# Performance work log

Hardware: AMD Instinct MI355X
Metric: run time of the kernel (lower is better)

The kernel has to match this reference:

```python
import jax, jax.numpy as jnp
import numpy as np

NUM_Q_HEADS = 32
NUM_KV_HEADS = 8
Q_GROUP = NUM_Q_HEADS // NUM_KV_HEADS
K_DIM = 128
V_DIM = 128
EMD_DIM = 4096
ROPE_BASE = 10000.0


def _rope_tables(seq_len, dim, offset=0, dtype=jnp.float32):
    # thetas: base**(-arange(0,dim,2)/dim); ticks tiled (1,2) -> [seq,dim]
    exps = -jnp.arange(0, dim, 2, dtype=jnp.float32) / dim
    thetas = ROPE_BASE ** exps
    t = jnp.arange(offset, offset + seq_len, dtype=jnp.float32)
    ticks = jnp.outer(t, thetas)                      # [t, dim/2]
    ticks = jnp.concatenate([ticks, ticks], axis=-1)  # tile (1,2) -> [t, dim]
    ticks = ticks[None, :, None, :]                   # [1, t, 1, dim]
    return jnp.cos(ticks).astype(dtype), jnp.sin(ticks).astype(dtype)


def _apply_rope(x, cos, sin):
    # x: [B, t, H, D]; rotate-half variant: neg_half = cat(-x2, x1)
    d2 = x.shape[-1] // 2
    x1, x2 = x[..., :d2], x[..., d2:]
    neg_half = jnp.concatenate([-x2, x1], axis=-1)
    return x * cos + neg_half * sin


def setup_inputs() -> dict:
    key = jax.random.key(0)
    ks = jax.random.split(key, 7)
    B, T, D = 2, 2048, EMD_DIM
    return {
        "q": jax.random.normal(ks[0], (B, T, D), dtype=jnp.float32),
        "k": jax.random.normal(ks[1], (B, T, D), dtype=jnp.float32),
        "v": jax.random.normal(ks[2], (B, T, D), dtype=jnp.float32),
        "wq": jax.random.normal(ks[3], (D, NUM_Q_HEADS * K_DIM), dtype=jnp.float32) * 0.02,
        "wk": jax.random.normal(ks[4], (D, NUM_KV_HEADS * K_DIM), dtype=jnp.float32) * 0.02,
        "wv": jax.random.normal(ks[5], (D, NUM_KV_HEADS * V_DIM), dtype=jnp.float32) * 0.02,
        "wo": jax.random.normal(ks[6], (Q_GROUP * NUM_KV_HEADS * V_DIM, D), dtype=jnp.float32) * 0.02,
    }


def reference(q, k, v, wq, wk, wv, wo):
    B, t, D = q.shape
    cos, sin = _rope_tables(t, K_DIM, offset=0, dtype=q.dtype)

    # projections + head split (no kv_cache -> offset 0, T == t)
    q_heads = jnp.einsum('btd,de->bte', q, wq).reshape(B, t, NUM_Q_HEADS, K_DIM)
    q_heads = _apply_rope(q_heads, cos, sin)
    k_heads = jnp.einsum('btd,de->bte', k, wk).reshape(B, t, NUM_KV_HEADS, K_DIM)
    k_heads = _apply_rope(k_heads, cos, sin)
    v_heads = jnp.einsum('btd,de->bte', v, wv).reshape(B, t, NUM_KV_HEADS, V_DIM)

    # grouped attention: [B, t, G, H, K] x [B, T, H, K] -> [B, G, H, t, T]
    gq = q_heads.reshape(B, t, Q_GROUP, NUM_KV_HEADS, K_DIM)
    scores = jnp.einsum('BtGHK,BTHK->BGHtT', gq, k_heads).astype(jnp.float32)
    causal = jnp.tril(jnp.ones((t, t), dtype=bool))
    scores = jnp.where(causal, scores, -jnp.inf)
    probs = jax.nn.softmax(scores / (K_DIM ** 0.5), axis=-1).astype(v_heads.dtype)

    out = jnp.einsum('BGHtT,BTHV->BtGHV', probs, v_heads)
    out = out.reshape(B, t, Q_GROUP * NUM_KV_HEADS * V_DIM)
    out = jnp.einsum('bti,io->bto', out, wo)

    new_kv_cache = jnp.concatenate([k_heads, v_heads], axis=-1)  # [B, T, H, K+V]
    return out, new_kv_cache
```

## Files before the change

kernel.cpp:

```cpp
#include <hip/hip_runtime.h>
#include <hip/hip_bf16.h>
#include <cstdint>
#include <math.h>

#define BB 2
#define TT 2048
#define DD 4096
#define HQ 32
#define HKV 8
#define DK 128
#define MM (BB*TT)
#define NQ (HQ*DK)
#define NKV (HKV*DK)

typedef __attribute__((ext_vector_type(8))) short short8;
typedef __attribute__((ext_vector_type(4))) short bshort4;
typedef __attribute__((ext_vector_type(4))) float floatx4;

typedef unsigned int u32;
typedef __attribute__((address_space(1))) const u32 gas_u32;
typedef __attribute__((address_space(3))) u32 las_u32;

__device__ __forceinline__ void gl_lds16(const uint16_t* g, uint16_t* l) {
    __builtin_amdgcn_global_load_lds((gas_u32*)g, (las_u32*)l, 16, 0, 0);
}

__device__ inline uint16_t f2bf(float f) {
    uint32_t u = __float_as_uint(f);
    uint32_t r = (u + 0x7fffu + ((u >> 16) & 1u)) >> 16;
    return (uint16_t)r;
}

__global__ void rope_tables_k(float* __restrict__ cosT, float* __restrict__ sinT) {
    int t = blockIdx.x;
    int d = threadIdx.x;
    float theta = expf(-(float)d * (9.210340371976184f / 64.0f));
    float arg = (float)t * theta;
    float s, c;
    sincosf(arg, &s, &c);
    cosT[t * 64 + d] = c;
    sinT[t * 64 + d] = s;
}

__global__ void wconv_k(const float* __restrict__ W, uint16_t* __restrict__ WT, int K, int N) {
    __shared__ float tile[32][33];
    int n0 = blockIdx.x * 32, k0 = blockIdx.y * 32;
    int tx = threadIdx.x, ty = threadIdx.y;
#pragma unroll
    for (int i = 0; i < 4; i++) {
        int r = k0 + ty + i * 8;
        tile[ty + i * 8][tx] = W[(size_t)r * N + n0 + tx];
    }
    __syncthreads();
#pragma unroll
    for (int i = 0; i < 4; i++) {
        int r = n0 + ty + i * 8;
        WT[(size_t)r * K + k0 + tx] = f2bf(tile[tx][ty + i * 8]);
    }
}

__global__ void aconv3_k(const float4* __restrict__ Xq, const float4* __restrict__ Xk,
                         const float4* __restrict__ Xv,
                         uint2* __restrict__ Yq, uint2* __restrict__ Yk, uint2* __restrict__ Yv,
                         int n4) {
    int i = blockIdx.x * blockDim.x + threadIdx.x;
    int w = blockIdx.y;
    const float4* X = (w == 0) ? Xq : (w == 1) ? Xk : Xv;
    uint2* Y = (w == 0) ? Yq : (w == 1) ? Yk : Yv;
    if (i < n4) {
        float4 v = X[i];
        uint2 o;
        o.x = (uint32_t)f2bf(v.x) | ((uint32_t)f2bf(v.y) << 16);
        o.y = (uint32_t)f2bf(v.z) | ((uint32_t)f2bf(v.w) << 16);
        Y[i] = o;
    }
}

__device__ __forceinline__ void gemm_core(
    const uint16_t* __restrict__ A, const uint16_t* __restrict__ Bm, int K,
    int m0, int n0, int tid, uint16_t* As, uint16_t* Bs, floatx4 acc[2][8])
{
    int lane = tid & 63, wave = tid >> 6;
    int l15 = lane & 15, quad = lane >> 4;
#pragma unroll
    for (int a = 0; a < 2; a++)
#pragma unroll
        for (int b = 0; b < 8; b++) acc[a][b] = floatx4{0.f, 0.f, 0.f, 0.f};

    int srow = tid >> 3;
    int skc = (tid & 7) ^ (srow & 7);
    const uint16_t* Ag = A + (size_t)(m0 + srow) * K + skc * 8;
    const uint16_t* Bg = Bm + (size_t)(n0 + srow) * K + skc * 8;
    uint16_t* Asl = As + tid * 8;
    uint16_t* Bsl = Bs + tid * 8;
    int rswA = l15 & 7;

    for (int k0 = 0; k0 < K; k0 += 64) {
        __syncthreads();
#pragma unroll
        for (int i = 0; i < 4; i++) {
            gl_lds16(Ag + (size_t)(i * 32) * K + k0, Asl + i * 2048);
            gl_lds16(Bg + (size_t)(i * 32) * K + k0, Bsl + i * 2048);
        }
        __syncthreads();
#pragma unroll
        for (int ks = 0; ks < 2; ks++) {
            short8 af[2], bfr[8];
#pragma unroll
            for (int mt = 0; mt < 2; mt++)
                af[mt] = *(const short8*)(As + (wave * 32 + mt * 16 + l15) * 64
                                             + (((ks << 2) | quad) ^ rswA) * 8);
#pragma unroll
            for (int nt = 0; nt < 8; nt++)
                bfr[nt] = *(const short8*)(Bs + (nt * 16 + l15) * 64
                                              + (((ks << 2) | quad) ^ rswA) * 8);
#pragma unroll
            for (int mt = 0; mt < 2; mt++)
#pragma unroll
                for (int nt = 0; nt < 8; nt++)
                    acc[mt][nt] = __builtin_amdgcn_mfma_f32_16x16x32_bf16(af[mt], bfr[nt], acc[mt][nt], 0, 0, 0);
        }
    }
}

template <int EPI>
__global__ __launch_bounds__(256) void gemm_k(
    const uint16_t* __restrict__ A, const uint16_t* __restrict__ Bm,
    int M, int N, int K,
    uint16_t* __restrict__ Obf, float* __restrict__ Ofp,
    const float* __restrict__ cosT, const float* __restrict__ sinT)
{
    __shared__ __attribute__((aligned(16))) uint16_t As[128 * 64];
    __shared__ __attribute__((aligned(16))) uint16_t Bs[128 * 64];
    int m0 = blockIdx.y * 128;
    int n0 = blockIdx.x * 128;
    int tid = threadIdx.x;
    int lane = tid & 63, wave = tid >> 6;
    int l15 = lane & 15, quad = lane >> 4;

    floatx4 acc[2][8];
    gemm_core(A, Bm, K, m0, n0, tid, As, Bs, acc);

#pragma unroll
    for (int mt = 0; mt < 2; mt++) {
        int rbase = m0 + wave * 32 + mt * 16 + quad * 4;
        if (EPI == 4) {
#pragma unroll
            for (int nt = 0; nt < 8; nt++) {
                int c = n0 + nt * 16 + l15;
#pragma unroll
                for (int r = 0; r < 4; r++)
                    Ofp[(size_t)(rbase + r) * N + c] = acc[mt][nt][r];
            }
        } else {
#pragma unroll
            for (int nt = 0; nt < 4; nt++) {
                int cb = nt * 16 + l15;
#pragma unroll
                for (int r = 0; r < 4; r++) {
                    int row = rbase + r;
                    int t = row & (TT - 1);
                    float cs = cosT[t * 64 + cb];
                    float sn = sinT[t * 64 + cb];
                    float x1 = acc[mt][nt][r], x2 = acc[mt][nt + 4][r];
                    float o1 = x1 * cs - x2 * sn;
                    float o2 = x2 * cs + x1 * sn;
                    Obf[(size_t)row * N + n0 + cb] = f2bf(o1);
                    Obf[(size_t)row * N + n0 + cb + 64] = f2bf(o2);
                }
            }
        }
    }
}

__global__ __launch_bounds__(256) void gemm_kv_k(
    const uint16_t* __restrict__ Akk, const uint16_t* __restrict__ Avv,
    const uint16_t* __restrict__ Wk, const uint16_t* __restrict__ Wv,
    uint16_t* __restrict__ khB, uint16_t* __restrict__ vhB, float* __restrict__ cache,
    const float* __restrict__ cosT, const float* __restrict__ sinT)
{
    __shared__ __attribute__((aligned(16))) uint16_t As[128 * 64];
    __shared__ __attribute__((aligned(16))) uint16_t Bs[128 * 64];
    bool isK = (blockIdx.z == 1);
    const uint16_t* A = isK ? Akk : Avv;
    const uint16_t* Bm = isK ? Wk : Wv;
    int m0 = blockIdx.y * 128;
    int n0 = blockIdx.x * 128;
    int tid = threadIdx.x;
    int lane = tid & 63, wave = tid >> 6;
    int l15 = lane & 15, quad = lane >> 4;

    floatx4 acc[2][8];
    gemm_core(A, Bm, DD, m0, n0, tid, As, Bs, acc);

    int h = n0 >> 7;
#pragma unroll
    for (int mt = 0; mt < 2; mt++) {
        int rbase = m0 + wave * 32 + mt * 16 + quad * 4;
        if (!isK) {
#pragma unroll
            for (int nt = 0; nt < 8; nt++) {
                int cb = nt * 16 + l15;
#pragma unroll
                for (int r = 0; r < 4; r++) {
                    int row = rbase + r;
                    float v = acc[mt][nt][r];
                    vhB[(size_t)row * NKV + n0 + cb] = f2bf(v);
                    cache[((size_t)row * 8 + h) * 256 + 128 + cb] = v;
                }
            }
        } else {
#pragma unroll
            for (int nt = 0; nt < 4; nt++) {
                int cb = nt * 16 + l15;
#pragma unroll
                for (int r = 0; r < 4; r++) {
                    int row = rbase + r;
                    int t = row & (TT - 1);
                    float cs = cosT[t * 64 + cb];
                    float sn = sinT[t * 64 + cb];
                    float x1 = acc[mt][nt][r], x2 = acc[mt][nt + 4][r];
                    float o1 = x1 * cs - x2 * sn;
                    float o2 = x2 * cs + x1 * sn;
                    khB[(size_t)row * NKV + n0 + cb] = f2bf(o1);
                    khB[(size_t)row * NKV + n0 + cb + 64] = f2bf(o2);
                    cache[((size_t)row * 8 + h) * 256 + cb] = o1;
                    cache[((size_t)row * 8 + h) * 256 + cb + 64] = o2;
                }
            }
        }
    }
}

__global__ void vtrans_k(const uint16_t* __restrict__ vh, uint16_t* __restrict__ vT) {
    __shared__ uint16_t tile[32][33];
    int bh = blockIdx.z;
    int t0 = blockIdx.x * 32;
    int d0 = blockIdx.y * 32;
    int b = bh >> 3, h = bh & 7;
    int tx = threadIdx.x, ty = threadIdx.y;
#pragma unroll
    for (int i = 0; i < 4; i++) {
        int t = t0 + ty + i * 8;
        tile[ty + i * 8][tx] = vh[(size_t)(b * TT + t) * NKV + h * DK + d0 + tx];
    }
    __syncthreads();
#pragma unroll
    for (int i = 0; i < 4; i++) {
        int d = d0 + ty + i * 8;
        vT[((size_t)bh * DK + d) * TT + t0 + tx] = tile[tx][ty + i * 8];
    }
}

__global__ __launch_bounds__(512, 4) void attn_k(
    const uint16_t* __restrict__ qh, const uint16_t* __restrict__ kh,
    const uint16_t* __restrict__ vT, uint16_t* __restrict__ ob)
{
    __shared__ __attribute__((aligned(16))) uint16_t Ks[32 * 136];
    __shared__ __attribute__((aligned(16))) uint16_t Vs[128 * 40];
    __shared__ __attribute__((aligned(16))) uint16_t Ps[8 * 16 * 40];

    int tid = threadIdx.x;
    int lane = tid & 63, wave = tid >> 6;
    int l15 = lane & 15, quad = lane >> 4;
    int sub = wave & 1, hg = wave >> 1;
    int kvh = blockIdx.y;
    int b = blockIdx.z;
    int hq = hg * 8 + kvh;
    uint16_t* P = Ps + wave * (16 * 40);

    const uint16_t* kbase = kh + (size_t)(b * TT) * NKV + kvh * DK;
    const uint16_t* vbase = vT + ((size_t)(b * 8 + kvh) * DK) * TT;
    const float scale2 = 0.08838834764831845f * 1.4426950408889634f;

    int kkey = tid >> 4, kdc = tid & 15;
    int vdv = tid >> 2, vtc = tid & 3;

    for (int half = 0; half < 2; half++) {
        int hh = half ? (63 - (int)blockIdx.x) : (int)blockIdx.x;
        int q0 = hh * 32;
        int ntiles = hh + 1;

        short8 qf[4];
        {
            const uint16_t* qr = qh + (size_t)(b * TT + q0 + sub * 16 + l15) * NQ + hq * DK;
#pragma unroll
            for (int ks = 0; ks < 4; ks++)
                qf[ks] = *(const short8*)(qr + ks * 32 + quad * 8);
        }

        floatx4 O[8];
#pragma unroll
        for (int vt = 0; vt < 8; vt++) O[vt] = floatx4{0.f, 0.f, 0.f, 0.f};
        float m_ = -INFINITY;
        float l_ = 0.f;

        short8 kst = *(const short8*)(kbase + (size_t)kkey * NKV + kdc * 8);
        short8 vst = *(const short8*)(vbase + (size_t)vdv * TT + vtc * 8);

        for (int t = 0; t < ntiles; t++) {
            int kb0 = t * 32;
            __syncthreads();
            *(short8*)(Ks + kkey * 136 + kdc * 8) = kst;
            *(short8*)(Vs + vdv * 40 + vtc * 8) = vst;
            __syncthreads();
            if (t + 1 < ntiles) {
                int kn = kb0 + 32;
                kst = *(const short8*)(kbase + (size_t)(kn + kkey) * NKV + kdc * 8);
                vst = *(const short8*)(vbase + (size_t)vdv * TT + kn + vtc * 8);
            }
            floatx4 s[2];
            s[0] = floatx4{0.f,0.f,0.f,0.f};
            s[1] = floatx4{0.f,0.f,0.f,0.f};
            __builtin_amdgcn_s_setprio(1);
#pragma unroll
            for (int ks = 0; ks < 4; ks++) {
                short8 kf0 = *(const short8*)(Ks + l15 * 136 + ks * 32 + quad * 8);
                short8 kf1 = *(const short8*)(Ks + (16 + l15) * 136 + ks * 32 + quad * 8);
                s[0] = __builtin_amdgcn_mfma_f32_16x16x32_bf16(kf0, qf[ks], s[0], 0, 0, 0);
                s[1] = __builtin_amdgcn_mfma_f32_16x16x32_bf16(kf1, qf[ks], s[1], 0, 0, 0);
            }
            __builtin_amdgcn_s_setprio(0);
            bool maskT = (t == ntiles - 1);
            int qrow = q0 + sub * 16 + l15;
            float p[8];
#pragma unroll
            for (int krt = 0; krt < 2; krt++)
#pragma unroll
                for (int r = 0; r < 4; r++) {
                    float v = s[krt][r] * scale2;
                    if (maskT && (kb0 + krt * 16 + quad * 4 + r > qrow)) v = -INFINITY;
                    p[krt * 4 + r] = v;
                }
            float mx = p[0];
#pragma unroll
            for (int j = 1; j < 8; j++) mx = fmaxf(mx, p[j]);
            mx = fmaxf(mx, __shfl_xor(mx, 16));
            mx = fmaxf(mx, __shfl_xor(mx, 32));
            bool noresc = (bool)__all(mx <= m_ + 8.0f);
            float mnew = noresc ? m_ : fmaxf(m_, mx);
            float e[8], sum = 0.f;
#pragma unroll
            for (int j = 0; j < 8; j++) { e[j] = exp2f(p[j] - mnew); sum += e[j]; }
            sum += __shfl_xor(sum, 16);
            sum += __shfl_xor(sum, 32);
            if (noresc) {
                l_ += sum;
            } else {
                float al = exp2f(m_ - mnew);
                l_ = l_ * al + sum;
                m_ = mnew;
                float ar[4];
#pragma unroll
                for (int r = 0; r < 4; r++) ar[r] = __shfl(al, quad * 4 + r);
#pragma unroll
                for (int vt = 0; vt < 8; vt++)
#pragma unroll
                    for (int r = 0; r < 4; r++) O[vt][r] *= ar[r];
            }
            bshort4 pw0, pw1;
#pragma unroll
            for (int r = 0; r < 4; r++) {
                pw0[r] = (short)((__float_as_uint(e[r]) + 0x8000u) >> 16);
                pw1[r] = (short)((__float_as_uint(e[4 + r]) + 0x8000u) >> 16);
            }
            *(bshort4*)(P + l15 * 40 + quad * 4) = pw0;
            *(bshort4*)(P + l15 * 40 + 16 + quad * 4) = pw1;
            short8 pf = *(const short8*)(P + l15 * 40 + quad * 8);
            __builtin_amdgcn_s_setprio(1);
#pragma unroll
            for (int vt = 0; vt < 8; vt++) {
                short8 vf = *(const short8*)(Vs + (vt * 16 + l15) * 40 + quad * 8);
                O[vt] = __builtin_amdgcn_mfma_f32_16x16x32_bf16(pf, vf, O[vt], 0, 0, 0);
            }
            __builtin_amdgcn_s_setprio(0);
        }
        float lr[4];
#pragma unroll
        for (int r = 0; r < 4; r++) lr[r] = 1.0f / __shfl(l_, quad * 4 + r);
#pragma unroll
        for (int r = 0; r < 4; r++) {
            size_t row = (size_t)(b * TT + q0 + sub * 16 + quad * 4 + r);
#pragma unroll
            for (int vt = 0; vt < 8; vt++)
                ob[row * NQ + hq * DK + vt * 16 + l15] = f2bf(O[vt][r] * lr[r]);
        }
    }
}

extern "C" void kernel_launch(void* const* d_in, const int* in_sizes, int n_in,
                              void* d_out, int out_size, void* d_ws, size_t ws_size,
                              hipStream_t stream)
{
    const float* q  = (const float*)d_in[0];
    const float* k  = (const float*)d_in[1];
    const float* v  = (const float*)d_in[2];
    const float* wq = (const float*)d_in[3];
    const float* wk = (const float*)d_in[4];
    const float* wv = (const float*)d_in[5];
    const float* wo = (const float*)d_in[6];
    float* out   = (float*)d_out;
    float* cache = out + (size_t)MM * DD;

    char* ws = (char*)d_ws;
    float* cosT = (float*)ws;
    float* sinT = cosT + TT * 64;
    size_t off = 1u << 20;
    const size_t SZ32 = (size_t)MM * DD * 2;
    const size_t SZ8  = (size_t)MM * NKV * 2;
    uint16_t* wqT = (uint16_t*)(ws + off); off += SZ32;
    uint16_t* wkT = (uint16_t*)(ws + off); off += SZ8;
    uint16_t* wvT = (uint16_t*)(ws + off); off += SZ8;
    uint16_t* qb  = (uint16_t*)(ws + off); off += SZ32;
    uint16_t* kb  = (uint16_t*)(ws + off); off += SZ32;
    uint16_t* vb  = (uint16_t*)(ws + off); off += SZ32;
    uint16_t* khB = (uint16_t*)(ws + off); off += SZ8;
    uint16_t* vhB = (uint16_t*)(ws + off); off += SZ8;
    uint16_t* vTr = wvT;
    uint16_t* qhB = vb;
    uint16_t* woT = kb;
    uint16_t* obf = qb;

    rope_tables_k<<<TT, 64, 0, stream>>>(cosT, sinT);
    wconv_k<<<dim3(NQ / 32, DD / 32), dim3(32, 8), 0, stream>>>(wq, wqT, DD, NQ);
    wconv_k<<<dim3(NKV / 32, DD / 32), dim3(32, 8), 0, stream>>>(wk, wkT, DD, NKV);
    wconv_k<<<dim3(NKV / 32, DD / 32), dim3(32, 8), 0, stream>>>(wv, wvT, DD, NKV);
    int n4 = MM * DD / 4;
    aconv3_k<<<dim3((n4 + 255) / 256, 3), 256, 0, stream>>>(
        (const float4*)q, (const float4*)k, (const float4*)v,
        (uint2*)qb, (uint2*)kb, (uint2*)vb, n4);
    gemm_kv_k<<<dim3(NKV / 128, MM / 128, 2), 256, 0, stream>>>(
        kb, vb, wkT, wvT, khB, vhB, cache, cosT, sinT);
    gemm_k<1><<<dim3(NQ / 128, MM / 128), 256, 0, stream>>>(qb, wqT, MM, NQ, DD, qhB, nullptr, cosT, sinT);
    wconv_k<<<dim3(DD / 32, DD / 32), dim3(32, 8), 0, stream>>>(wo, woT, DD, DD);
    vtrans_k<<<dim3(TT / 32, DK / 32, BB * HKV), dim3(32, 8), 0, stream>>>(vhB, vTr);
    attn_k<<<dim3(32, HKV, BB), 512, 0, stream>>>(qhB, khB, vTr, obf);
    gemm_k<4><<<dim3(DD / 128, MM / 128), 256, 0, stream>>>(obf, woT, MM, DD, DD, nullptr, out, cosT, sinT);
}
```

Measured before the change: 937.1 us.

## Switch projection GEMMs to 256x256 double-buffered tiles with block swizzle

Replaces the 128x128 single-buffered GEMM core with a 256x256 tile, 512-thread kernel that double-buffers LDS, prefetching the next K slice with direct global-to-LDS loads while computing the current one. It also uses manual waitcnt/barrier control, MFMA priority bumps and an L2-friendly block index swizzle. Wq/Wk rows are permuted at conversion so each wave's 64-column slice holds matching RoPE halves for the epilogue. The larger tile uses 128KB of LDS and many accumulator registers, which limits occupancy and gives fewer blocks for the smaller KV GEMM.

After: 887.9 us. 1.06x faster.

```diff
diff --git a/kernel.cpp b/kernel.cpp
--- a/kernel.cpp
+++ b/kernel.cpp
@@ -31,6 +31,20 @@
     return (uint16_t)r;
 }
 
+#define ASM_VMCNT8 asm volatile("s_waitcnt vmcnt(8)" ::: "memory")
+#define ASM_VMCNT0 asm volatile("s_waitcnt vmcnt(0)" ::: "memory")
+#define ASM_LGKM0  asm volatile("s_waitcnt lgkmcnt(0)" ::: "memory")
+#define RAW_BAR    __builtin_amdgcn_s_barrier()
+#define SCHED_B    __builtin_amdgcn_sched_barrier(0)
+
+__device__ __forceinline__ void swz_xy(int gx, int nwg, int& bx, int& by) {
+    int idx = by * gx + bx;
+    int cpx = nwg >> 3;
+    idx = (idx & 7) * cpx + (idx >> 3);
+    bx = idx % gx;
+    by = idx / gx;
+}
+
 __global__ void rope_tables_k(float* __restrict__ cosT, float* __restrict__ sinT) {
     int t = blockIdx.x;
     int d = threadIdx.x;
@@ -42,6 +56,7 @@
     sinT[t * 64 + d] = s;
 }
 
+template <bool PERM>
 __global__ void wconv_k(const float* __restrict__ W, uint16_t* __restrict__ WT, int K, int N) {
     __shared__ float tile[32][33];
     int n0 = blockIdx.x * 32, k0 = blockIdx.y * 32;
@@ -55,7 +70,9 @@
 #pragma unroll
     for (int i = 0; i < 4; i++) {
         int r = n0 + ty + i * 8;
-        WT[(size_t)r * K + k0 + tx] = f2bf(tile[tx][ty + i * 8]);
+        int rp = r;
+        if (PERM) rp = (r & ~96) | (((r >> 5) & 1) << 6) | (((r >> 6) & 1) << 5);
+        WT[(size_t)rp * K + k0 + tx] = f2bf(tile[tx][ty + i * 8]);
     }
 }
 
@@ -76,159 +93,231 @@
     }
 }
 
-__device__ __forceinline__ void gemm_core(
+__device__ __forceinline__ void gemm256_core(
     const uint16_t* __restrict__ A, const uint16_t* __restrict__ Bm, int K,
-    int m0, int n0, int tid, uint16_t* As, uint16_t* Bs, floatx4 acc[2][8])
+    int m0, int n0, int tid, uint16_t* As2, uint16_t* Bs2, floatx4 acc[8][4])
 {
-    int lane = tid & 63, wave = tid >> 6;
+    int lane = tid & 63;
     int l15 = lane & 15, quad = lane >> 4;
-#pragma unroll
-    for (int a = 0; a < 2; a++)
-#pragma unroll
-        for (int b = 0; b < 8; b++) acc[a][b] = floatx4{0.f, 0.f, 0.f, 0.f};
+    int wave = tid >> 6;
+    int wm = wave >> 2, wn = wave & 3;
+
+#pragma unroll
+    for (int a = 0; a < 8; a++)
+#pragma unroll
+        for (int b = 0; b < 4; b++) acc[a][b] = floatx4{0.f, 0.f, 0.f, 0.f};
 
     int srow = tid >> 3;
     int skc = (tid & 7) ^ (srow & 7);
-    const uint16_t* Ag = A + (size_t)(m0 + srow) * K + skc * 8;
-    const uint16_t* Bg = Bm + (size_t)(n0 + srow) * K + skc * 8;
-    uint16_t* Asl = As + tid * 8;
-    uint16_t* Bsl = Bs + tid * 8;
-    int rswA = l15 & 7;
-
-    for (int k0 = 0; k0 < K; k0 += 64) {
-        __syncthreads();
-#pragma unroll
-        for (int i = 0; i < 4; i++) {
-            gl_lds16(Ag + (size_t)(i * 32) * K + k0, Asl + i * 2048);
-            gl_lds16(Bg + (size_t)(i * 32) * K + k0, Bsl + i * 2048);
+    const uint16_t* Ab = A + (size_t)(m0 + srow) * K + skc * 8;
+    const uint16_t* Bb = Bm + (size_t)(n0 + srow) * K + skc * 8;
+    uint16_t* AsD = As2 + tid * 8;
+    uint16_t* BsD = Bs2 + tid * 8;
+    int rsw = l15 & 7;
+
+    const int NT = K / 64;
+
+#pragma unroll
+    for (int i = 0; i < 4; i++) {
+        gl_lds16(Ab + (size_t)(i * 64) * K, AsD + i * 4096);
+        gl_lds16(Bb + (size_t)(i * 64) * K, BsD + i * 4096);
+    }
+
+    for (int t = 0; t < NT; ++t) {
+        const uint16_t* bufA = As2 + (t & 1) * 16384;
+        const uint16_t* bufB = Bs2 + (t & 1) * 16384;
+        ASM_LGKM0;
+        SCHED_B;
+        RAW_BAR;
+        SCHED_B;
+        if (t + 1 < NT) {
+            int k0n = (t + 1) * 64;
+            uint16_t* dA = As2 + ((t + 1) & 1) * 16384 + tid * 8;
+            uint16_t* dB = Bs2 + ((t + 1) & 1) * 16384 + tid * 8;
+#pragma unroll
+            for (int i = 0; i < 4; i++) {
+                gl_lds16(Ab + (size_t)(i * 64) * K + k0n, dA + i * 4096);
+                gl_lds16(Bb + (size_t)(i * 64) * K + k0n, dB + i * 4096);
+            }
+            ASM_VMCNT8;
+        } else {
+            ASM_VMCNT0;
         }
-        __syncthreads();
-#pragma unroll
-        for (int ks = 0; ks < 2; ks++) {
-            short8 af[2], bfr[8];
-#pragma unroll
-            for (int mt = 0; mt < 2; mt++)
-                af[mt] = *(const short8*)(As + (wave * 32 + mt * 16 + l15) * 64
-                                             + (((ks << 2) | quad) ^ rswA) * 8);
-#pragma unroll
-            for (int nt = 0; nt < 8; nt++)
-                bfr[nt] = *(const short8*)(Bs + (nt * 16 + l15) * 64
-                                              + (((ks << 2) | quad) ^ rswA) * 8);
-#pragma unroll
-            for (int mt = 0; mt < 2; mt++)
-#pragma unroll
-                for (int nt = 0; nt < 8; nt++)
-                    acc[mt][nt] = __builtin_amdgcn_mfma_f32_16x16x32_bf16(af[mt], bfr[nt], acc[mt][nt], 0, 0, 0);
+        SCHED_B;
+        RAW_BAR;
+        SCHED_B;
+
+#pragma unroll
+        for (int qm = 0; qm < 2; qm++) {
+            short8 af[4][2];
+#pragma unroll
+            for (int fm = 0; fm < 4; fm++)
+#pragma unroll
+                for (int ks = 0; ks < 2; ks++) {
+                    int row = wm * 128 + qm * 64 + fm * 16 + l15;
+                    af[fm][ks] = *(const short8*)(bufA + row * 64 + ((((ks << 2) | quad) ^ rsw) << 3));
+                }
+#pragma unroll
+            for (int qn = 0; qn < 2; qn++) {
+                short8 bfv[2][2];
+#pragma unroll
+                for (int fn = 0; fn < 2; fn++)
+#pragma unroll
+                    for (int ks = 0; ks < 2; ks++) {
+                        int row = wn * 64 + qn * 32 + fn * 16 + l15;
+                        bfv[fn][ks] = *(const short8*)(bufB + row * 64 + ((((ks << 2) | quad) ^ rsw) << 3));
+                    }
+                __builtin_amdgcn_s_setprio(1);
+#pragma unroll
+                for (int ks = 0; ks < 2; ks++)
+#pragma unroll
+                    for (int fm = 0; fm < 4; fm++)
+#pragma unroll
+                        for (int fn = 0; fn < 2; fn++)
+                            acc[qm * 4 + fm][qn * 2 + fn] = __builtin_amdgcn_mfma_f32_16x16x32_bf16(
+                                af[fm][ks], bfv[fn][ks], acc[qm * 4 + fm][qn * 2 + fn], 0, 0, 0);
+                __builtin_amdgcn_s_setprio(0);
+            }
         }
     }
 }
 
 template <int EPI>
-__global__ __launch_bounds__(256) void gemm_k(
+__global__ __launch_bounds__(512, 2) void gemm256_k(
     const uint16_t* __restrict__ A, const uint16_t* __restrict__ Bm,
     int M, int N, int K,
     uint16_t* __restrict__ Obf, float* __restrict__ Ofp,
     const float* __restrict__ cosT, const float* __restrict__ sinT)
 {
-    __shared__ __attribute__((aligned(16))) uint16_t As[128 * 64];
-    __shared__ __attribute__((aligned(16))) uint16_t Bs[128 * 64];
-    int m0 = blockIdx.y * 128;
-    int n0 = blockIdx.x * 128;
+    __shared__ __attribute__((aligned(16))) uint16_t AB[4 * 16384];
+    int bx = blockIdx.x, by = blockIdx.y;
+    swz_xy(gridDim.x, gridDim.x * gridDim.y, bx, by);
+    int m0 = by * 256, n0 = bx * 256;
     int tid = threadIdx.x;
     int lane = tid & 63, wave = tid >> 6;
     int l15 = lane & 15, quad = lane >> 4;
-
-    floatx4 acc[2][8];
-    gemm_core(A, Bm, K, m0, n0, tid, As, Bs, acc);
-
-#pragma unroll
-    for (int mt = 0; mt < 2; mt++) {
-        int rbase = m0 + wave * 32 + mt * 16 + quad * 4;
-        if (EPI == 4) {
-#pragma unroll
-            for (int nt = 0; nt < 8; nt++) {
-                int c = n0 + nt * 16 + l15;
-#pragma unroll
-                for (int r = 0; r < 4; r++)
-                    Ofp[(size_t)(rbase + r) * N + c] = acc[mt][nt][r];
-            }
-        } else {
-#pragma unroll
-            for (int nt = 0; nt < 4; nt++) {
-                int cb = nt * 16 + l15;
-#pragma unroll
-                for (int r = 0; r < 4; r++) {
-                    int row = rbase + r;
-                    int t = row & (TT - 1);
-                    float cs = cosT[t * 64 + cb];
-                    float sn = sinT[t * 64 + cb];
-                    float x1 = acc[mt][nt][r], x2 = acc[mt][nt + 4][r];
-                    float o1 = x1 * cs - x2 * sn;
-                    float o2 = x2 * cs + x1 * sn;
-                    Obf[(size_t)row * N + n0 + cb] = f2bf(o1);
-                    Obf[(size_t)row * N + n0 + cb + 64] = f2bf(o2);
+    int wm = wave >> 2, wn = wave & 3;
+
+    floatx4 acc[8][4];
+    gemm256_core(A, Bm, K, m0, n0, tid, AB, AB + 2 * 16384, acc);
+
+    if (EPI == 4) {
+#pragma unroll
+        for (int qm = 0; qm < 2; qm++)
+#pragma unroll
+            for (int fm = 0; fm < 4; fm++) {
+                int rbase = m0 + wm * 128 + qm * 64 + fm * 16 + quad * 4;
+#pragma unroll
+                for (int qn = 0; qn < 2; qn++)
+#pragma unroll
+                    for (int fn = 0; fn < 2; fn++) {
+                        int c = n0 + wn * 64 + qn * 32 + fn * 16 + l15;
+#pragma unroll
+                        for (int r = 0; r < 4; r++)
+                            Ofp[(size_t)(rbase + r) * N + c] = acc[qm * 4 + fm][qn * 2 + fn][r];
+                    }
+            }
+    } else {
+        int c64 = n0 + wn * 64;
+        int h = c64 >> 7;
+        int j = (c64 >> 6) & 1;
+#pragma unroll
+        for (int qm = 0; qm < 2; qm++)
+#pragma unroll
+            for (int fm = 0; fm < 4; fm++) {
+                int rbase = m0 + wm * 128 + qm * 64 + fm * 16 + quad * 4;
+#pragma unroll
+                for (int fn = 0; fn < 2; fn++) {
+                    int d = j * 32 + fn * 16 + l15;
+#pragma unroll
+                    for (int r = 0; r < 4; r++) {
+                        int row = rbase + r;
+                        int t = row & (TT - 1);
+                        float cs = cosT[t * 64 + d];
+                        float sn = sinT[t * 64 + d];
+                        float x1 = acc[qm * 4 + fm][fn][r];
+                        float x2 = acc[qm * 4 + fm][2 + fn][r];
+                        float o1 = x1 * cs - x2 * sn;
+                        float o2 = x2 * cs + x1 * sn;
+                        Obf[(size_t)row * N + h * 128 + d] = f2bf(o1);
+                        Obf[(size_t)row * N + h * 128 + d + 64] = f2bf(o2);
+                    }
                 }
             }
-        }
-    }
-}
-
-__global__ __launch_bounds__(256) void gemm_kv_k(
+    }
+}
+
+__global__ __launch_bounds__(512, 2) void gemm256_kv_k(
     const uint16_t* __restrict__ Akk, const uint16_t* __restrict__ Avv,
     const uint16_t* __restrict__ Wk, const uint16_t* __restrict__ Wv,
     uint16_t* __restrict__ khB, uint16_t* __restrict__ vhB, float* __restrict__ cache,
     const float* __restrict__ cosT, const float* __restrict__ sinT)
 {
-    __shared__ __attribute__((aligned(16))) uint16_t As[128 * 64];
-    __shared__ __attribute__((aligned(16))) uint16_t Bs[128 * 64];
+    __shared__ __attribute__((aligned(16))) uint16_t AB[4 * 16384];
     bool isK = (blockIdx.z == 1);
     const uint16_t* A = isK ? Akk : Avv;
     const uint16_t* Bm = isK ? Wk : Wv;
-    int m0 = blockIdx.y * 128;
-    int n0 = blockIdx.x * 128;
+    int bx = blockIdx.x, by = blockIdx.y;
+    swz_xy(gridDim.x, gridDim.x * gridDim.y, bx, by);
+    int m0 = by * 256, n0 = bx * 256;
     int tid = threadIdx.x;
     int lane = tid & 63, wave = tid >> 6;
     int l15 = lane & 15, quad = lane >> 4;
-
-    floatx4 acc[2][8];
-    gemm_core(A, Bm, DD, m0, n0, tid, As, Bs, acc);
-
-    int h = n0 >> 7;
-#pragma unroll
-    for (int mt = 0; mt < 2; mt++) {
-        int rbase = m0 + wave * 32 + mt * 16 + quad * 4;
-        if (!isK) {
-#pragma unroll
-            for (int nt = 0; nt < 8; nt++) {
-                int cb = nt * 16 + l15;
-#pragma unroll
-                for (int r = 0; r < 4; r++) {
-                    int row = rbase + r;
-                    float v = acc[mt][nt][r];
-                    vhB[(size_t)row * NKV + n0 + cb] = f2bf(v);
-                    cache[((size_t)row * 8 + h) * 256 + 128 + cb] = v;
+    int wm = wave >> 2, wn = wave & 3;
+
+    floatx4 acc[8][4];
+    gemm256_core(A, Bm, DD, m0, n0, tid, AB, AB + 2 * 16384, acc);
+
+    if (!isK) {
+#pragma unroll
+        for (int qm = 0; qm < 2; qm++)
+#pragma unroll
+            for (int fm = 0; fm < 4; fm++) {
+                int rbase = m0 + wm * 128 + qm * 64 + fm * 16 + quad * 4;
+#pragma unroll
+                for (int qn = 0; qn < 2; qn++)
+#pragma unroll
+                    for (int fn = 0; fn < 2; fn++) {
+                        int c = n0 + wn * 64 + qn * 32 + fn * 16 + l15;
+                        int h = c >> 7, cb = c & 127;
+#pragma unroll
+                        for (int r = 0; r < 4; r++) {
+                            int row = rbase + r;
+                            float v = acc[qm * 4 + fm][qn * 2 + fn][r];
+                            vhB[(size_t)row * NKV + c] = f2bf(v);
+                            cache[((size_t)row * 8 + h) * 256 + 128 + cb] = v;
+                        }
+                    }
+            }
+    } else {
+        int c64 = n0 + wn * 64;
+        int h = c64 >> 7;
+        int j = (c64 >> 6) & 1;
+#pragma unroll
+        for (int qm = 0; qm < 2; qm++)
+#pragma unroll
+            for (int fm = 0; fm < 4; fm++) {
+                int rbase = m0 + wm * 128 + qm * 64 + fm * 16 + quad * 4;
+#pragma unroll
+                for (int fn = 0; fn < 2; fn++) {
+                    int d = j * 32 + fn * 16 + l15;
+#pragma unroll
+                    for (int r = 0; r < 4; r++) {
+                        int row = rbase + r;
+                        int t = row & (TT - 1);
+                        float cs = cosT[t * 64 + d];
+                        float sn = sinT[t * 64 + d];
+                        float x1 = acc[qm * 4 + fm][fn][r];
+                        float x2 = acc[qm * 4 + fm][2 + fn][r];
+                        float o1 = x1 * cs - x2 * sn;
+                        float o2 = x2 * cs + x1 * sn;
+                        khB[(size_t)row * NKV + h * 128 + d] = f2bf(o1);
+                        khB[(size_t)row * NKV + h * 128 + d + 64] = f2bf(o2);
+                        cache[((size_t)row * 8 + h) * 256 + d] = o1;
+                        cache[((size_t)row * 8 + h) * 256 + d + 64] = o2;
+                    }
                 }
             }
-        } else {
-#pragma unroll
-            for (int nt = 0; nt < 4; nt++) {
-                int cb = nt * 16 + l15;
-#pragma unroll
-                for (int r = 0; r < 4; r++) {
-                    int row = rbase + r;
-                    int t = row & (TT - 1);
-                    float cs = cosT[t * 64 + cb];
-                    float sn = sinT[t * 64 + cb];
-                    float x1 = acc[mt][nt][r], x2 = acc[mt][nt + 4][r];
-                    float o1 = x1 * cs - x2 * sn;
-                    float o2 = x2 * cs + x1 * sn;
-                    khB[(size_t)row * NKV + n0 + cb] = f2bf(o1);
-                    khB[(size_t)row * NKV + n0 + cb + 64] = f2bf(o2);
-                    cache[((size_t)row * 8 + h) * 256 + cb] = o1;
-                    cache[((size_t)row * 8 + h) * 256 + cb + 64] = o2;
-                }
-            }
-        }
     }
 }
 
@@ -422,18 +511,18 @@
     uint16_t* obf = qb;
 
     rope_tables_k<<<TT, 64, 0, stream>>>(cosT, sinT);
-    wconv_k<<<dim3(NQ / 32, DD / 32), dim3(32, 8), 0, stream>>>(wq, wqT, DD, NQ);
-    wconv_k<<<dim3(NKV / 32, DD / 32), dim3(32, 8), 0, stream>>>(wk, wkT, DD, NKV);
-    wconv_k<<<dim3(NKV / 32, DD / 32), dim3(32, 8), 0, stream>>>(wv, wvT, DD, NKV);
+    wconv_k<true><<<dim3(NQ / 32, DD / 32), dim3(32, 8), 0, stream>>>(wq, wqT, DD, NQ);
+    wconv_k<true><<<dim3(NKV / 32, DD / 32), dim3(32, 8), 0, stream>>>(wk, wkT, DD, NKV);
+    wconv_k<false><<<dim3(NKV / 32, DD / 32), dim3(32, 8), 0, stream>>>(wv, wvT, DD, NKV);
     int n4 = MM * DD / 4;
     aconv3_k<<<dim3((n4 + 255) / 256, 3), 256, 0, stream>>>(
         (const float4*)q, (const float4*)k, (const float4*)v,
         (uint2*)qb, (uint2*)kb, (uint2*)vb, n4);
-    gemm_kv_k<<<dim3(NKV / 128, MM / 128, 2), 256, 0, stream>>>(
+    gemm256_kv_k<<<dim3(NKV / 256, MM / 256, 2), 512, 0, stream>>>(
         kb, vb, wkT, wvT, khB, vhB, cache, cosT, sinT);
-    gemm_k<1><<<dim3(NQ / 128, MM / 128), 256, 0, stream>>>(qb, wqT, MM, NQ, DD, qhB, nullptr, cosT, sinT);
-    wconv_k<<<dim3(DD / 32, DD / 32), dim3(32, 8), 0, stream>>>(wo, woT, DD, DD);
+    gemm256_k<1><<<dim3(NQ / 256, MM / 256), 512, 0, stream>>>(qb, wqT, MM, NQ, DD, qhB, nullptr, cosT, sinT);
+    wconv_k<false><<<dim3(DD / 32, DD / 32), dim3(32, 8), 0, stream>>>(wo, woT, DD, DD);
     vtrans_k<<<dim3(TT / 32, DK / 32, BB * HKV), dim3(32, 8), 0, stream>>>(vhB, vTr);
     attn_k<<<dim3(32, HKV, BB), 512, 0, stream>>>(qhB, khB, vTr, obf);
-    gemm_k<4><<<dim3(DD / 128, MM / 128), 256, 0, stream>>>(obf, woT, MM, DD, DD, nullptr, out, cosT, sinT);
-}
+    gemm256_k<4><<<dim3(DD / 256, MM / 256), 512, 0, stream>>>(obf, woT, MM, DD, DD, nullptr, out, cosT, sinT);
+}
```
